# Kernel tuning notes

Hardware: AMD Instinct MI355X
Metric: run time of the kernel (lower is better)

Reference implementation:

```python
import jax, jax.numpy as jnp
import numpy as np

B, S, C, H = 2, 4096, 1024, 8
D = C // H
KCONV = 7  # depthwise causal conv kernel size


def setup_inputs() -> dict:
    key = jax.random.key(0)
    k1, k2, k3, k4 = jax.random.split(key, 4)
    x = jax.random.normal(k1, (B, S, C), jnp.float32)
    Wqkv = jax.random.normal(k2, (C, 3 * C), jnp.float32) * (1.0 / np.sqrt(C))
    Wo = jax.random.normal(k3, (C, C), jnp.float32) * (1.0 / np.sqrt(C))
    conv_w = jax.random.normal(k4, (C, KCONV), jnp.float32) * (1.0 / np.sqrt(KCONV))
    return {"x": x, "Wqkv": Wqkv, "Wo": Wo, "conv_w": conv_w}


def _ripple(x, Wqkv, Wo, conv_w):
    b, s, c = x.shape
    d = c // H
    qkv = x @ Wqkv
    q, k, v = jnp.split(qkv, 3, axis=-1)

    def heads(t):
        return t.reshape(b, s, H, d).transpose(0, 2, 1, 3)  # [B,H,S,D]

    qh, kh, vh = heads(q), heads(k), heads(v)

    # --- branch 1: telescoping attention (offsets 0, 1, 2, 4, ..., 2^k) ---
    n_pow = int(np.floor(np.log2(s))) + 1
    offsets = jnp.concatenate([jnp.zeros((1,), jnp.int32),
                               (2 ** jnp.arange(n_pow)).astype(jnp.int32)])  # [K]
    pos = jnp.arange(s, dtype=jnp.int32)[:, None] - offsets[None, :]  # [S,K]
    valid = pos >= 0
    posc = jnp.clip(pos, 0)
    kg = kh[:, :, posc]  # [B,H,S,K,D] gathered keys
    vg = vh[:, :, posc]  # [B,H,S,K,D] gathered values
    sc = jnp.einsum('bhsd,bhskd->bhsk', qh, kg) / np.sqrt(d)
    sc = jnp.where(valid[None, None], sc, -jnp.inf)  # offset 0 always valid
    w = jax.nn.softmax(sc, axis=-1)
    tele = jnp.einsum('bhsk,bhskd->bhsd', w, vg)

    # --- branch 2: depthwise causal conv over value stream ---
    vpad = jnp.pad(v, ((0, 0), (KCONV - 1, 0), (0, 0)))  # left pad -> causal
    conv = jax.lax.conv_general_dilated(
        vpad.transpose(0, 2, 1),        # NCH
        conv_w[:, None, :],             # OIH, groups=C -> I=1
        window_strides=(1,), padding='VALID',
        feature_group_count=c,
        dimension_numbers=('NCH', 'OIH', 'NCH')).transpose(0, 2, 1)  # [B,S,C]
    conv_h = conv.reshape(b, s, H, d).transpose(0, 2, 1, 3)

    # --- branch 3: low-rank (linear) attention, elu+1 feature map ---
    fq = jax.nn.elu(qh) + 1.0
    fk = jax.nn.elu(kh) + 1.0
    kv = jnp.einsum('bhsd,bhse->bhde', fk, vh)        # [B,H,D,D]
    z = jnp.einsum('bhsd,bhd->bhs', fq, fk.sum(2))    # normalizer
    low = jnp.einsum('bhsd,bhde->bhse', fq, kv) / (z[..., None] + 1e-6)

    h = (tele + conv_h + low).transpose(0, 2, 1, 3).reshape(b, s, c)
    return h @ Wo


def reference(x, Wqkv, Wo, conv_w):
    # RippleAttentionBlock: h, _ = ripple_attn(x); return x + h
    return x + _ripple(x, Wqkv, Wo, conv_w)
```

## Files before the change

kernel.cpp:

```cpp
#include <hip/hip_runtime.h>
#include <hip/hip_bf16.h>

#define BATCH 2
#define SEQ   4096
#define CHN   1024
#define NH    8
#define HD    128
#define NQROWS (BATCH*SEQ)
#define QKVN  (3*CHN)
#define NOFF  14
#define KCONV 7
#define NCH   16
#define CHS   (SEQ/NCH)

typedef short bf16x8v __attribute__((ext_vector_type(8)));
typedef short bf16x4v __attribute__((ext_vector_type(4)));
typedef float f32x4v  __attribute__((ext_vector_type(4)));

__device__ __forceinline__ float b2f(short s) {
    return __uint_as_float(((unsigned)(unsigned short)s) << 16);
}
__device__ __forceinline__ unsigned short f2bu(float f) {
    __hip_bfloat16 h = __float2bfloat16(f);
    return *reinterpret_cast<unsigned short*>(&h);
}
__device__ __forceinline__ void gload16(const void* g, void* l) {
    __builtin_amdgcn_global_load_lds(
        (const __attribute__((address_space(1))) unsigned int*)g,
        (__attribute__((address_space(3))) unsigned int*)l, 16, 0, 0);
}

__global__ void k_cvt(const float* __restrict__ in, short* __restrict__ out, int n4) {
    int i = blockIdx.x * blockDim.x + threadIdx.x;
    int stride = gridDim.x * blockDim.x;
    for (; i < n4; i += stride) {
        float4 v = reinterpret_cast<const float4*>(in)[i];
        ushort4 o;
        o.x = f2bu(v.x); o.y = f2bu(v.y); o.z = f2bu(v.z); o.w = f2bu(v.w);
        reinterpret_cast<ushort4*>(out)[i] = o;
    }
}

__global__ void k_transpose_cvt(const float* __restrict__ in, short* __restrict__ out,
                                int R, int Cc) {
    __shared__ float tile[32][33];
    int bc = blockIdx.x * 32, br = blockIdx.y * 32;
    int tx = threadIdx.x & 31, ty = threadIdx.x >> 5;
    for (int i = 0; i < 32; i += 8)
        tile[ty + i][tx] = in[(size_t)(br + ty + i) * Cc + bc + tx];
    __syncthreads();
    for (int i = 0; i < 32; i += 8)
        out[(size_t)(bc + ty + i) * R + br + tx] = (short)f2bu(tile[tx][ty + i]);
}

template<int EPI>
__global__ __launch_bounds__(256)
void k_gemm_bt(const short* __restrict__ A, const short* __restrict__ Bt,
               short* __restrict__ Cb, float* __restrict__ Cf,
               const float* __restrict__ resid, int M, int N, int K) {
    __shared__ short As[128 * 32];
    __shared__ short Bs[128 * 32];
    int tid = threadIdx.x;
    int w = tid >> 6, lane = tid & 63;
    int nbn = N >> 7;
    int bm = blockIdx.x / nbn, bn = blockIdx.x % nbn;
    size_t m0 = (size_t)bm << 7, n0 = (size_t)bn << 7;
    int wr = (w >> 1) << 6, wc = (w & 1) << 6;
    int lr = lane & 15, lk = lane >> 4;
    f32x4v acc[4][4] = {};

    int f0 = w * 64 + lane, f1 = f0 + 256;
    int r0 = f0 >> 2, q0 = f0 & 3;
    int r1 = f1 >> 2, q1 = f1 & 3;
    const short* Ap0 = A + (m0 + r0) * K + q0 * 8;
    const short* Ap1 = A + (m0 + r1) * K + q1 * 8;
    const short* Bp0 = Bt + (n0 + r0) * K + q0 * 8;
    const short* Bp1 = Bt + (n0 + r1) * K + q1 * 8;
    short* Asl0 = As + (w * 64) * 8;
    short* Asl1 = As + (256 + w * 64) * 8;
    short* Bsl0 = Bs + (w * 64) * 8;
    short* Bsl1 = Bs + (256 + w * 64) * 8;

    for (int k0 = 0; k0 < K; k0 += 32) {
        gload16(Ap0 + k0, Asl0);
        gload16(Ap1 + k0, Asl1);
        gload16(Bp0 + k0, Bsl0);
        gload16(Bp1 + k0, Bsl1);
        __syncthreads();
        bf16x8v af[4], bfv[4];
        #pragma unroll
        for (int m = 0; m < 4; ++m)
            af[m] = *reinterpret_cast<const bf16x8v*>(As + (wr + m * 16 + lr) * 32 + lk * 8);
        #pragma unroll
        for (int n = 0; n < 4; ++n)
            bfv[n] = *reinterpret_cast<const bf16x8v*>(Bs + (wc + n * 16 + lr) * 32 + lk * 8);
        #pragma unroll
        for (int m = 0; m < 4; ++m)
            #pragma unroll
            for (int n = 0; n < 4; ++n)
                acc[m][n] = __builtin_amdgcn_mfma_f32_16x16x32_bf16(af[m], bfv[n], acc[m][n], 0, 0, 0);
        __syncthreads();
    }
    #pragma unroll
    for (int m = 0; m < 4; ++m) {
        size_t grow = m0 + wr + m * 16 + lk * 4;
        #pragma unroll
        for (int n = 0; n < 4; ++n) {
            size_t gcol = n0 + wc + n * 16 + lr;
            #pragma unroll
            for (int i = 0; i < 4; ++i) {
                size_t idx = (grow + i) * N + gcol;
                if (EPI == 0) Cb[idx] = (short)f2bu(acc[m][n][i]);
                else          Cf[idx] = resid[idx] + acc[m][n][i];
            }
        }
    }
}

__global__ __launch_bounds__(256)
void k_kvpart(const short* __restrict__ qkv, float* __restrict__ kvpart,
              float* __restrict__ kspart) {
    __shared__ float fk_lds[32 * 128];
    __shared__ short v_lds[32 * 64];
    int t = threadIdx.x;
    int w = t >> 6, lane = t & 63;
    int bid = blockIdx.x;
    int eh = bid & 1;
    int ch = (bid >> 1) & (NCH - 1);
    int bh = bid / (NCH * 2);
    int b = bh >> 3, h = bh & 7;
    size_t rowbase = (size_t)b * SEQ + (size_t)ch * CHS;
    const short* kbase = qkv + CHN + h * HD;
    const short* vbase = qkv + 2 * CHN + h * HD + eh * 64;
    int d0 = (t >> 4) * 8;
    int e0l = (t & 15) * 4;
    float kv[8][4] = {};
    float ks[8] = {};
    for (int sub = 0; sub < CHS / 32; ++sub) {
        #pragma unroll
        for (int j = 0; j < 2; ++j) {
            int f = j * 256 + t;
            int row = f >> 4, c0 = (f & 15) * 8;
            bf16x8v k8 = *reinterpret_cast<const bf16x8v*>(
                kbase + (rowbase + sub * 32 + row) * QKVN + c0);
            float* dst = fk_lds + row * 128 + c0;
            #pragma unroll
            for (int e = 0; e < 8; ++e) {
                float x = b2f(k8[e]);
                dst[e] = x > 0.f ? x + 1.f : __expf(x);
            }
        }
        {
            int f = w * 64 + lane;
            gload16(vbase + (rowbase + sub * 32 + (f >> 3)) * QKVN + (f & 7) * 8,
                    v_lds + (size_t)(w * 64) * 8);
        }
        __syncthreads();
        for (int ss = 0; ss < 32; ++ss) {
            float fa[8];
            *(float4*)&fa[0] = *(const float4*)&fk_lds[ss * 128 + d0];
            *(float4*)&fa[4] = *(const float4*)&fk_lds[ss * 128 + d0 + 4];
            bf16x4v vv = *reinterpret_cast<const bf16x4v*>(&v_lds[ss * 64 + e0l]);
            float vb[4];
            #pragma unroll
            for (int e = 0; e < 4; ++e) vb[e] = b2f(vv[e]);
            #pragma unroll
            for (int i = 0; i < 8; ++i) {
                ks[i] += fa[i];
                #pragma unroll
                for (int e = 0; e < 4; ++e) kv[i][e] += fa[i] * vb[e];
            }
        }
        __syncthreads();
    }
    size_t obase = (size_t)bid * (128 * 64);
    #pragma unroll
    for (int i = 0; i < 8; ++i)
        *(float4*)&kvpart[obase + (d0 + i) * 64 + e0l] = *(float4*)&kv[i][0];
    if ((t & 15) == 0 && eh == 0)
        #pragma unroll
        for (int i = 0; i < 8; ++i)
            kspart[(size_t)(bh * NCH + ch) * 128 + d0 + i] = ks[i];
}

__global__ void k_kvreduce(const float* __restrict__ kvpart, const float* __restrict__ kspart,
                           short* __restrict__ kvt, float* __restrict__ ksum) {
    int idx = blockIdx.x * blockDim.x + threadIdx.x;
    const int total_kv = 16 * 128 * 128;
    if (idx < total_kv) {
        int bh = idx >> 14;
        int r = idx & 16383;
        int d = r >> 7, e = r & 127;
        int ehalf = e >> 6, el = e & 63;
        float s = 0.f;
        const float* p = kvpart + ((size_t)(bh * NCH) * 2 + ehalf) * 8192 + d * 64 + el;
        #pragma unroll
        for (int c = 0; c < NCH; ++c) s += p[(size_t)c * 2 * 8192];
        kvt[((size_t)bh << 14) + e * 128 + d] = (short)f2bu(s);
    } else {
        int k = idx - total_kv;
        if (k < 16 * 128) {
            int bh = k >> 7, d = k & 127;
            float s = 0.f;
            const float* p = kspart + (size_t)bh * NCH * 128 + d;
            #pragma unroll
            for (int c = 0; c < NCH; ++c) s += p[c * 128];
            ksum[k] = s;
        }
    }
}

__global__ __launch_bounds__(256)
void k_middle(const short* __restrict__ qkv, const short* __restrict__ kvt,
              const float* __restrict__ ksum, const float* __restrict__ conv_w,
              short* __restrict__ hbuf) {
    __shared__ short fq_lds[32 * 128];
    __shared__ float low_lds[32 * 128];
    __shared__ float ksum_lds[128];
    __shared__ float cw_lds[128 * KCONV];
    int t = threadIdx.x;
    int w = t >> 6, lane = t & 63;
    int bid = blockIdx.x;
    int bh = bid >> 7, chunk = bid & 127;
    int b = bh >> 3, h = bh & 7;
    int s0 = chunk * 32;
    size_t rowbase = (size_t)b * SEQ;
    const short* qbase = qkv + h * HD;
    const short* kbase = qkv + CHN + h * HD;
    const short* vbase = qkv + 2 * CHN + h * HD;

    if (t < 128) ksum_lds[t] = ksum[bh * 128 + t];
    for (int f = t; f < 128 * KCONV; f += 256) {
        int d = f / KCONV, j = f % KCONV;
        cw_lds[f] = conv_w[(h * HD + d) * KCONV + j];
    }
    #pragma unroll
    for (int j = 0; j < 2; ++j) {
        int f = j * 256 + t;
        int row = f >> 4, c0 = (f & 15) * 8;
        bf16x8v q8 = *reinterpret_cast<const bf16x8v*>(
            qbase + (rowbase + s0 + row) * QKVN + c0);
        bf16x8v fq8;
        #pragma unroll
        for (int e = 0; e < 8; ++e) {
            float x = b2f(q8[e]);
            float fx = x > 0.f ? x + 1.f : __expf(x);
            fq8[e] = (short)f2bu(fx);
        }
        *reinterpret_cast<bf16x8v*>(fq_lds + row * 128 + c0) = fq8;
    }
    __syncthreads();
    {
        int lr = lane & 15, lk = lane >> 4;
        const short* kvg = kvt + ((size_t)bh << 14);
        f32x4v lacc[2][2] = {};
        #pragma unroll
        for (int ksb = 0; ksb < 4; ++ksb) {
            bf16x8v af[2], bfv[2];
            #pragma unroll
            for (int m = 0; m < 2; ++m)
                af[m] = *reinterpret_cast<const bf16x8v*>(fq_lds + (m * 16 + lr) * 128 + ksb * 32 + lk * 8);
            #pragma unroll
            for (int n = 0; n < 2; ++n)
                bfv[n] = *reinterpret_cast<const bf16x8v*>(kvg + (w * 32 + n * 16 + lr) * 128 + ksb * 32 + lk * 8);
            #pragma unroll
            for (int m = 0; m < 2; ++m)
                #pragma unroll
                for (int n = 0; n < 2; ++n)
                    lacc[m][n] = __builtin_amdgcn_mfma_f32_16x16x32_bf16(af[m], bfv[n], lacc[m][n], 0, 0, 0);
        }
        #pragma unroll
        for (int m = 0; m < 2; ++m)
            #pragma unroll
            for (int n = 0; n < 2; ++n)
                #pragma unroll
                for (int i = 0; i < 4; ++i)
                    low_lds[(m * 16 + lk * 4 + i) * 128 + w * 32 + n * 16 + lr] = lacc[m][n][i];
    }
    int row = t >> 3, j8 = t & 7;
    int e0 = j8 * 16;
    int sl = s0 + row;
    float zp = 0.f;
    #pragma unroll
    for (int d = 0; d < 16; ++d)
        zp += b2f(fq_lds[row * 128 + e0 + d]) * ksum_lds[e0 + d];
    zp += __shfl_xor(zp, 1); zp += __shfl_xor(zp, 2); zp += __shfl_xor(zp, 4);
    float z = zp + 1e-6f;
    float qv[16];
    {
        const short* qp = qbase + (rowbase + sl) * QKVN + e0;
        bf16x8v q0 = *(const bf16x8v*)qp;
        bf16x8v q1 = *(const bf16x8v*)(qp + 8);
        #pragma unroll
        for (int d = 0; d < 8; ++d) { qv[d] = b2f(q0[d]); qv[8 + d] = b2f(q1[d]); }
    }
    float scb[NOFF];
    #pragma unroll
    for (int o = 0; o < NOFF; ++o) {
        int off = (o == 0) ? 0 : (1 << (o - 1));
        int p = sl - off;
        float acc = 0.f;
        if (p >= 0) {
            const short* kp = kbase + (rowbase + p) * QKVN + e0;
            bf16x8v k0v = *(const bf16x8v*)kp;
            bf16x8v k1v = *(const bf16x8v*)(kp + 8);
            #pragma unroll
            for (int d = 0; d < 8; ++d) acc += qv[d] * b2f(k0v[d]);
            #pragma unroll
            for (int d = 0; d < 8; ++d) acc += qv[8 + d] * b2f(k1v[d]);
        }
        scb[o] = acc;
    }
    #pragma unroll
    for (int o = 0; o < NOFF; ++o) {
        float v = scb[o];
        v += __shfl_xor(v, 1); v += __shfl_xor(v, 2); v += __shfl_xor(v, 4);
        scb[o] = v * 0.08838834764831845f;
    }
    float mmax = -1e30f;
    #pragma unroll
    for (int o = 0; o < NOFF; ++o) {
        int off = (o == 0) ? 0 : (1 << (o - 1));
        if (sl - off >= 0 && scb[o] > mmax) mmax = scb[o];
    }
    float wsum = 0.f;
    float tacc[16] = {};
    #pragma unroll
    for (int o = 0; o < NOFF; ++o) {
        int off = (o == 0) ? 0 : (1 << (o - 1));
        int p = sl - off;
        if (p < 0) continue;
        float wv = __expf(scb[o] - mmax);
        wsum += wv;
        const short* vp = vbase + (rowbase + p) * QKVN + e0;
        bf16x8v v0 = *(const bf16x8v*)vp;
        bf16x8v v1 = *(const bf16x8v*)(vp + 8);
        #pragma unroll
        for (int d = 0; d < 8; ++d) tacc[d]     += wv * b2f(v0[d]);
        #pragma unroll
        for (int d = 0; d < 8; ++d) tacc[8 + d] += wv * b2f(v1[d]);
    }
    float inv_wsum = 1.f / wsum;
    float cacc[16] = {};
    #pragma unroll
    for (int jj = 0; jj < KCONV; ++jj) {
        int p = sl - 6 + jj;
        if (p < 0) continue;
        const short* vp = vbase + (rowbase + p) * QKVN + e0;
        bf16x8v v0 = *(const bf16x8v*)vp;
        bf16x8v v1 = *(const bf16x8v*)(vp + 8);
        #pragma unroll
        for (int d = 0; d < 8; ++d) cacc[d]     += b2f(v0[d]) * cw_lds[(e0 + d) * KCONV + jj];
        #pragma unroll
        for (int d = 0; d < 8; ++d) cacc[8 + d] += b2f(v1[d]) * cw_lds[(e0 + 8 + d) * KCONV + jj];
    }
    __syncthreads();
    short outv[16];
    #pragma unroll
    for (int d = 0; d < 16; ++d) {
        float hval = tacc[d] * inv_wsum + cacc[d] + low_lds[row * 128 + e0 + d] / z;
        outv[d] = (short)f2bu(hval);
    }
    bf16x8v* op = (bf16x8v*)(hbuf + (rowbase + sl) * CHN + h * HD + e0);
    op[0] = *(bf16x8v*)&outv[0];
    op[1] = *(bf16x8v*)&outv[8];
}

extern "C" void kernel_launch(void* const* d_in, const int* in_sizes, int n_in,
                              void* d_out, int out_size, void* d_ws, size_t ws_size,
                              hipStream_t stream) {
    const float* x      = (const float*)d_in[0];
    const float* Wqkv   = (const float*)d_in[1];
    const float* Wo     = (const float*)d_in[2];
    const float* conv_w = (const float*)d_in[3];
    float* out = (float*)d_out;

    char* ws = (char*)d_ws;
    size_t off = 0;
    auto alloc = [&](size_t bytes) {
        char* p = ws + off;
        off += (bytes + 255) & ~(size_t)255;
        return (void*)p;
    };
    short* xb     = (short*)alloc((size_t)NQROWS * CHN * 2);
    short* wqkvT  = (short*)alloc((size_t)QKVN * CHN * 2);
    short* woT    = (short*)alloc((size_t)CHN * CHN * 2);
    short* qkv    = (short*)alloc((size_t)NQROWS * QKVN * 2);
    short* hbuf   = (short*)alloc((size_t)NQROWS * CHN * 2);
    float* kvpart = (float*)alloc((size_t)16 * NCH * 2 * 128 * 64 * 4);
    float* kspart = (float*)alloc((size_t)16 * NCH * 128 * 4);
    short* kvt    = (short*)alloc((size_t)16 * 128 * 128 * 2);
    float* ksum   = (float*)alloc((size_t)16 * 128 * 4);

    k_cvt<<<2048, 256, 0, stream>>>(x, xb, NQROWS * CHN / 4);
    k_transpose_cvt<<<dim3(QKVN / 32, CHN / 32), 256, 0, stream>>>(Wqkv, wqkvT, CHN, QKVN);
    k_transpose_cvt<<<dim3(CHN / 32, CHN / 32), 256, 0, stream>>>(Wo, woT, CHN, CHN);
    k_gemm_bt<0><<<(NQROWS / 128) * (QKVN / 128), 256, 0, stream>>>(
        xb, wqkvT, qkv, nullptr, nullptr, NQROWS, QKVN, CHN);
    k_kvpart<<<16 * NCH * 2, 256, 0, stream>>>(qkv, kvpart, kspart);
    k_kvreduce<<<(16 * 128 * 128 + 16 * 128) / 256, 256, 0, stream>>>(kvpart, kspart, kvt, ksum);
    k_middle<<<16 * 128, 256, 0, stream>>>(qkv, kvt, ksum, conv_w, hbuf);
    k_gemm_bt<1><<<(NQROWS / 128) * (CHN / 128), 256, 0, stream>>>(
        hbuf, woT, nullptr, out, x, NQROWS, CHN, CHN);
}
```

Before: 297.6 us.

## Store QKV in head-major [3,B,H,S,D] layout from GEMM epilogue

```diff
diff --git a/kernel.cpp b/kernel.cpp
--- a/kernel.cpp
+++ b/kernel.cpp
@@ -12,6 +12,7 @@
 #define KCONV 7
 #define NCH   16
 #define CHS   (SEQ/NCH)
+#define SLICE ((size_t)SEQ*HD)
 
 typedef short bf16x8v __attribute__((ext_vector_type(8)));
 typedef short bf16x4v __attribute__((ext_vector_type(4)));
@@ -107,18 +108,30 @@
         #pragma unroll
         for (int n = 0; n < 4; ++n) {
             size_t gcol = n0 + wc + n * 16 + lr;
-            #pragma unroll
-            for (int i = 0; i < 4; ++i) {
-                size_t idx = (grow + i) * N + gcol;
-                if (EPI == 0) Cb[idx] = (short)f2bu(acc[m][n][i]);
-                else          Cf[idx] = resid[idx] + acc[m][n][i];
+            if (EPI == 0) {
+                int bq = (int)(grow >> 12);
+                int tq = (int)(gcol >> 10);
+                int hh = ((int)gcol >> 7) & 7;
+                int d  = (int)gcol & 127;
+                size_t base = ((size_t)(tq * 2 + bq) * 8 + hh) * SLICE + d;
+                #pragma unroll
+                for (int i = 0; i < 4; ++i) {
+                    size_t s = (grow + i) & 4095;
+                    Cb[base + s * 128] = (short)f2bu(acc[m][n][i]);
+                }
+            } else {
+                #pragma unroll
+                for (int i = 0; i < 4; ++i) {
+                    size_t idx = (grow + i) * N + gcol;
+                    Cf[idx] = resid[idx] + acc[m][n][i];
+                }
             }
         }
     }
 }
 
 __global__ __launch_bounds__(256)
-void k_kvpart(const short* __restrict__ qkv, float* __restrict__ kvpart,
+void k_kvpart(const short* __restrict__ qkvs, float* __restrict__ kvpart,
               float* __restrict__ kspart) {
     __shared__ float fk_lds[32 * 128];
     __shared__ short v_lds[32 * 64];
@@ -129,9 +142,9 @@
     int ch = (bid >> 1) & (NCH - 1);
     int bh = bid / (NCH * 2);
     int b = bh >> 3, h = bh & 7;
-    size_t rowbase = (size_t)b * SEQ + (size_t)ch * CHS;
-    const short* kbase = qkv + CHN + h * HD;
-    const short* vbase = qkv + 2 * CHN + h * HD + eh * 64;
+    const short* kbase = qkvs + ((size_t)(2 + b) * 8 + h) * SLICE;
+    const short* vbase = qkvs + ((size_t)(4 + b) * 8 + h) * SLICE + eh * 64;
+    int s0 = ch * CHS;
     int d0 = (t >> 4) * 8;
     int e0l = (t & 15) * 4;
     float kv[8][4] = {};
@@ -142,7 +155,7 @@
             int f = j * 256 + t;
             int row = f >> 4, c0 = (f & 15) * 8;
             bf16x8v k8 = *reinterpret_cast<const bf16x8v*>(
-                kbase + (rowbase + sub * 32 + row) * QKVN + c0);
+                kbase + (size_t)(s0 + sub * 32 + row) * HD + c0);
             float* dst = fk_lds + row * 128 + c0;
             #pragma unroll
             for (int e = 0; e < 8; ++e) {
@@ -152,7 +165,7 @@
         }
         {
             int f = w * 64 + lane;
-            gload16(vbase + (rowbase + sub * 32 + (f >> 3)) * QKVN + (f & 7) * 8,
+            gload16(vbase + (size_t)(s0 + sub * 32 + (f >> 3)) * HD + (f & 7) * 8,
                     v_lds + (size_t)(w * 64) * 8);
         }
         __syncthreads();
@@ -211,7 +224,7 @@
 }
 
 __global__ __launch_bounds__(256)
-void k_middle(const short* __restrict__ qkv, const short* __restrict__ kvt,
+void k_middle(const short* __restrict__ qkvs, const short* __restrict__ kvt,
               const float* __restrict__ ksum, const float* __restrict__ conv_w,
               short* __restrict__ hbuf) {
     __shared__ short fq_lds[32 * 128];
@@ -224,10 +237,9 @@
     int bh = bid >> 7, chunk = bid & 127;
     int b = bh >> 3, h = bh & 7;
     int s0 = chunk * 32;
-    size_t rowbase = (size_t)b * SEQ;
-    const short* qbase = qkv + h * HD;
-    const short* kbase = qkv + CHN + h * HD;
-    const short* vbase = qkv + 2 * CHN + h * HD;
+    const short* qbase = qkvs + ((size_t)(0 + b) * 8 + h) * SLICE;
+    const short* kbase = qkvs + ((size_t)(2 + b) * 8 + h) * SLICE;
+    const short* vbase = qkvs + ((size_t)(4 + b) * 8 + h) * SLICE;
 
     if (t < 128) ksum_lds[t] = ksum[bh * 128 + t];
     for (int f = t; f < 128 * KCONV; f += 256) {
@@ -239,7 +251,7 @@
         int f = j * 256 + t;
         int row = f >> 4, c0 = (f & 15) * 8;
         bf16x8v q8 = *reinterpret_cast<const bf16x8v*>(
-            qbase + (rowbase + s0 + row) * QKVN + c0);
+            qbase + (size_t)(s0 + row) * HD + c0);
         bf16x8v fq8;
         #pragma unroll
         for (int e = 0; e < 8; ++e) {
@@ -288,7 +300,7 @@
     float z = zp + 1e-6f;
     float qv[16];
     {
-        const short* qp = qbase + (rowbase + sl) * QKVN + e0;
+        const short* qp = qbase + (size_t)sl * HD + e0;
         bf16x8v q0 = *(const bf16x8v*)qp;
         bf16x8v q1 = *(const bf16x8v*)(qp + 8);
         #pragma unroll
@@ -301,7 +313,7 @@
         int p = sl - off;
         float acc = 0.f;
         if (p >= 0) {
-            const short* kp = kbase + (rowbase + p) * QKVN + e0;
+            const short* kp = kbase + (size_t)p * HD + e0;
             bf16x8v k0v = *(const bf16x8v*)kp;
             bf16x8v k1v = *(const bf16x8v*)(kp + 8);
             #pragma unroll
@@ -332,7 +344,7 @@
         if (p < 0) continue;
         float wv = __expf(scb[o] - mmax);
         wsum += wv;
-        const short* vp = vbase + (rowbase + p) * QKVN + e0;
+        const short* vp = vbase + (size_t)p * HD + e0;
         bf16x8v v0 = *(const bf16x8v*)vp;
         bf16x8v v1 = *(const bf16x8v*)(vp + 8);
         #pragma unroll
@@ -346,7 +358,7 @@
     for (int jj = 0; jj < KCONV; ++jj) {
         int p = sl - 6 + jj;
         if (p < 0) continue;
-        const short* vp = vbase + (rowbase + p) * QKVN + e0;
+        const short* vp = vbase + (size_t)p * HD + e0;
         bf16x8v v0 = *(const bf16x8v*)vp;
         bf16x8v v1 = *(const bf16x8v*)(vp + 8);
         #pragma unroll
@@ -361,7 +373,7 @@
         float hval = tacc[d] * inv_wsum + cacc[d] + low_lds[row * 128 + e0 + d] / z;
         outv[d] = (short)f2bu(hval);
     }
-    bf16x8v* op = (bf16x8v*)(hbuf + (rowbase + sl) * CHN + h * HD + e0);
+    bf16x8v* op = (bf16x8v*)(hbuf + ((size_t)b * SEQ + sl) * CHN + h * HD + e0);
     op[0] = *(bf16x8v*)&outv[0];
     op[1] = *(bf16x8v*)&outv[8];
 }
@@ -385,7 +397,7 @@
     short* xb     = (short*)alloc((size_t)NQROWS * CHN * 2);
     short* wqkvT  = (short*)alloc((size_t)QKVN * CHN * 2);
     short* woT    = (short*)alloc((size_t)CHN * CHN * 2);
-    short* qkv    = (short*)alloc((size_t)NQROWS * QKVN * 2);
+    short* qkvs   = (short*)alloc((size_t)3 * BATCH * NH * SEQ * HD * 2);
     short* hbuf   = (short*)alloc((size_t)NQROWS * CHN * 2);
     float* kvpart = (float*)alloc((size_t)16 * NCH * 2 * 128 * 64 * 4);
     float* kspart = (float*)alloc((size_t)16 * NCH * 128 * 4);
@@ -396,10 +408,10 @@
     k_transpose_cvt<<<dim3(QKVN / 32, CHN / 32), 256, 0, stream>>>(Wqkv, wqkvT, CHN, QKVN);
     k_transpose_cvt<<<dim3(CHN / 32, CHN / 32), 256, 0, stream>>>(Wo, woT, CHN, CHN);
     k_gemm_bt<0><<<(NQROWS / 128) * (QKVN / 128), 256, 0, stream>>>(
-        xb, wqkvT, qkv, nullptr, nullptr, NQROWS, QKVN, CHN);
-    k_kvpart<<<16 * NCH * 2, 256, 0, stream>>>(qkv, kvpart, kspart);
+        xb, wqkvT, qkvs, nullptr, nullptr, NQROWS, QKVN, CHN);
+    k_kvpart<<<16 * NCH * 2, 256, 0, stream>>>(qkvs, kvpart, kspart);
     k_kvreduce<<<(16 * 128 * 128 + 16 * 128) / 256, 256, 0, stream>>>(kvpart, kspart, kvt, ksum);
-    k_middle<<<16 * 128, 256, 0, stream>>>(qkv, kvt, ksum, conv_w, hbuf);
+    k_middle<<<16 * 128, 256, 0, stream>>>(qkvs, kvt, ksum, conv_w, hbuf);
     k_gemm_bt<1><<<(NQROWS / 128) * (CHN / 128), 256, 0, stream>>>(
         hbuf, woT, nullptr, out, x, NQROWS, CHN, CHN);
 }
```

After: 298.9 us. Within noise of the previous version (+0.4%).
